# Kernel tuning notes

Measured on AMD Instinct MI355X. Metric: run time of the kernel, lower is better.

The kernel has to match this reference:

```python
import jax, jax.numpy as jnp
import numpy as np

FACTOR = 1.0

def _dct_matrix():
    n = 8
    D = np.zeros((n * n, n * n), dtype=np.float32)
    for u in range(n):
        for v in range(n):
            au = 1.0 / np.sqrt(2.0) if u == 0 else 1.0
            av = 1.0 / np.sqrt(2.0) if v == 0 else 1.0
            alpha = au * av * 0.25
            for x in range(n):
                for y in range(n):
                    D[u * n + v, x * n + y] = alpha * np.cos((2 * x + 1) * u * np.pi / 16) * np.cos((2 * y + 1) * v * np.pi / 16)
    return D

def _y_quant_table():
    t = np.array([[16, 11, 10, 16, 24, 40, 51, 61], [12, 12, 14, 19, 26, 58, 60, 55],
                  [14, 13, 16, 24, 40, 57, 69, 56], [14, 17, 22, 29, 51, 87, 80, 62],
                  [18, 22, 37, 56, 68, 109, 103, 77], [24, 35, 55, 64, 81, 104, 113, 92],
                  [49, 64, 78, 87, 103, 121, 120, 101], [72, 92, 95, 98, 112, 100, 103, 99]],
                 dtype=np.float32).T
    return t

def _c_quant_table():
    t = np.full((8, 8), 99, dtype=np.float32)
    t[:4, :4] = np.array([[17, 18, 24, 47], [18, 21, 26, 66], [24, 26, 56, 99], [47, 66, 99, 99]],
                          dtype=np.float32).T
    return t

_D = jnp.asarray(_dct_matrix())          # [64,64]
_QT = jnp.stack([jnp.asarray(_y_quant_table()),
                 jnp.asarray(_c_quant_table()),
                 jnp.asarray(_c_quant_table())], axis=0) * FACTOR  # [3,8,8]

def setup_inputs() -> dict:
    key = jax.random.key(0)
    image = jax.random.uniform(key, (32, 3, 512, 512), dtype=jnp.float32)
    return {"image": image}

def _diffjpeg(image):
    x = jnp.clip(image, 0.0, 1.0)
    B, C, H, W = x.shape  # H, W multiples of 8 -> no padding branch
    r, g, b = x[:, 0], x[:, 1], x[:, 2]
    y = 0.299 * r + 0.587 * g + 0.114 * b
    cb = (b - y) * 0.564 + 0.5
    cr = (r - y) * 0.713 + 0.5
    ycbcr = jnp.stack([y, cb, cr], axis=1)  # [B,3,H,W]
    # blockify into 8x8 tiles
    nh, nw = H // 8, W // 8
    blocks = ycbcr.reshape(B, C, nh, 8, nw, 8).transpose(0, 1, 2, 4, 3, 5)  # [B,C,nh,nw,8,8]
    flat = blocks.reshape(-1, 64) * 255.0 - 128.0
    dct = flat @ _D.T                      # matmul(D, flat.T).T
    dctb = dct.reshape(B, C, nh, nw, 8, 8)
    qte = _QT[None, :, None, None, :, :]   # [1,3,1,1,8,8]
    q = dctb / qte
    q = q + jax.lax.stop_gradient(jnp.round(q) - q)  # STE rounding
    deq = q * qte
    idct = deq.reshape(-1, 64) @ _D        # matmul(D.T, x.T).T
    idct = (idct + 128.0) / 255.0
    img = idct.reshape(B, C, nh, nw, 8, 8).transpose(0, 1, 2, 4, 3, 5).reshape(B, C, H, W)
    yy, ycb, ycr = img[:, 0], img[:, 1] - 0.5, img[:, 2] - 0.5
    rr = yy + 1.403 * ycr
    gg = yy - 0.714 * ycr - 0.344 * ycb
    bb = yy + 1.773 * ycb
    rgb = jnp.clip(jnp.stack([rr, gg, bb], axis=1), 0.0, 1.0)
    return jnp.clip(rgb, 0.0, 1.0)

def reference(image):
    return _diffjpeg(image)
```

## Files before the change

kernel.cpp:

```cpp
#include <hip/hip_runtime.h>

#define K4 0.353553391f
#define K1 0.490392640f
#define K3 0.415734806f
#define K5 0.277785117f
#define K7 0.097545161f
#define K2 0.461939766f
#define K6 0.191341716f

__device__ __align__(16) const float YQT[64] = {
    16.f, 12.f, 14.f, 14.f,  18.f,  24.f,  49.f,  72.f,
    11.f, 12.f, 13.f, 17.f,  22.f,  35.f,  64.f,  92.f,
    10.f, 14.f, 16.f, 22.f,  37.f,  55.f,  78.f,  95.f,
    16.f, 19.f, 24.f, 29.f,  56.f,  64.f,  87.f,  98.f,
    24.f, 26.f, 40.f, 51.f,  68.f,  81.f, 103.f, 112.f,
    40.f, 58.f, 57.f, 87.f, 109.f, 104.f, 121.f, 100.f,
    51.f, 60.f, 69.f, 80.f, 103.f, 113.f, 120.f, 103.f,
    61.f, 55.f, 56.f, 62.f,  77.f,  92.f, 101.f,  99.f
};

__device__ __align__(16) const float CQ[64] = {
    17.f, 18.f, 24.f, 47.f, 99.f, 99.f, 99.f, 99.f,
    18.f, 21.f, 26.f, 66.f, 99.f, 99.f, 99.f, 99.f,
    24.f, 26.f, 56.f, 99.f, 99.f, 99.f, 99.f, 99.f,
    47.f, 66.f, 99.f, 99.f, 99.f, 99.f, 99.f, 99.f,
    99.f, 99.f, 99.f, 99.f, 99.f, 99.f, 99.f, 99.f,
    99.f, 99.f, 99.f, 99.f, 99.f, 99.f, 99.f, 99.f,
    99.f, 99.f, 99.f, 99.f, 99.f, 99.f, 99.f, 99.f,
    99.f, 99.f, 99.f, 99.f, 99.f, 99.f, 99.f, 99.f
};

__device__ __forceinline__ void dct8(const float x[8], float X[8]) {
    const float a0 = x[0] + x[7], a1 = x[1] + x[6], a2 = x[2] + x[5], a3 = x[3] + x[4];
    const float d0 = x[0] - x[7], d1 = x[1] - x[6], d2 = x[2] - x[5], d3 = x[3] - x[4];
    const float e0 = a0 + a3, e1 = a1 + a2, f0 = a0 - a3, f1 = a1 - a2;
    X[0] = K4 * (e0 + e1);
    X[4] = K4 * (e0 - e1);
    X[2] = K2 * f0 + K6 * f1;
    X[6] = K6 * f0 - K2 * f1;
    X[1] = K1 * d0 + K3 * d1 + K5 * d2 + K7 * d3;
    X[3] = K3 * d0 - K7 * d1 - K1 * d2 - K5 * d3;
    X[5] = K5 * d0 - K1 * d1 + K7 * d2 + K3 * d3;
    X[7] = K7 * d0 - K5 * d1 + K3 * d2 - K1 * d3;
}

__device__ __forceinline__ void idct8(const float X[8], float x[8]) {
    const float g0 = K4 * (X[0] + X[4]);
    const float g1 = K4 * (X[0] - X[4]);
    const float E0 = g0 + K2 * X[2] + K6 * X[6];
    const float E1 = g1 + K6 * X[2] - K2 * X[6];
    const float E2 = g1 - K6 * X[2] + K2 * X[6];
    const float E3 = g0 - K2 * X[2] - K6 * X[6];
    const float O0 = K1 * X[1] + K3 * X[3] + K5 * X[5] + K7 * X[7];
    const float O1 = K3 * X[1] - K7 * X[3] - K1 * X[5] - K5 * X[7];
    const float O2 = K5 * X[1] - K1 * X[3] + K7 * X[5] + K3 * X[7];
    const float O3 = K7 * X[1] - K5 * X[3] + K3 * X[5] - K1 * X[7];
    x[0] = E0 + O0;  x[7] = E0 - O0;
    x[1] = E1 + O1;  x[6] = E1 - O1;
    x[2] = E2 + O2;  x[5] = E2 - O2;
    x[3] = E3 + O3;  x[4] = E3 - O3;
}

__device__ __forceinline__ void wave_lds_fence() {
    asm volatile("s_waitcnt lgkmcnt(0)" ::: "memory");
}

#define LDSW 68

__global__ __launch_bounds__(256, 6) void diffjpeg_kernel(const float* __restrict__ in,
                                                          float* __restrict__ out)
{
    __shared__ __align__(16) float pl[3][32][LDSW];

    const int t  = threadIdx.x;
    const int l  = t & 63;
    const int wv = t >> 6;
    const int r0 = wv * 8;

    const int bid  = blockIdx.x;
    const int img  = bid >> 7;
    const int rem  = bid & 127;
    const int trow = rem >> 3;
    const int tcol = rem & 7;
    const size_t HW = (size_t)512 * 512;
    const size_t sbase = (size_t)img * 3 * HW + (size_t)(trow * 32 + wv * 8) * 512 + (size_t)(tcol * 64);
    const float* __restrict__ pin  = in  + sbase;
    float* __restrict__       pout = out + sbase;

    {
        const float* cb = pin + l;
        float rv[8], gv[8], bv[8];
        #pragma unroll
        for (int x = 0; x < 8; ++x) rv[x] = cb[(size_t)x * 512];
        #pragma unroll
        for (int x = 0; x < 8; ++x) gv[x] = cb[HW + (size_t)x * 512];
        #pragma unroll
        for (int x = 0; x < 8; ++x) bv[x] = cb[2 * HW + (size_t)x * 512];

        float yv[8], cbv[8], crv[8];
        #pragma unroll
        for (int x = 0; x < 8; ++x) {
            const float r = fminf(fmaxf(rv[x], 0.f), 1.f);
            const float g = fminf(fmaxf(gv[x], 0.f), 1.f);
            const float b = fminf(fmaxf(bv[x], 0.f), 1.f);
            const float Y = fmaf(76.245f, r, fmaf(149.685f, g, 29.07f * b));
            yv[x]  = Y - 128.f;
            cbv[x] = fmaf(0.564f, fmaf(255.f, b, -Y), -0.5f);
            crv[x] = fmaf(0.713f, fmaf(255.f, r, -Y), -0.5f);
        }

        float X0[8], X1[8], X2[8];
        dct8(yv,  X0);
        dct8(cbv, X1);
        dct8(crv, X2);
        #pragma unroll
        for (int u = 0; u < 8; ++u) {
            pl[0][r0 + u][l] = X0[u];
            pl[1][r0 + u][l] = X1[u];
            pl[2][r0 + u][l] = X2[u];
        }
    }
    wave_lds_fence();

    {
        const int b8 = (l >> 3) * 8;
        const int rr = l & 7;

        const float4* yq4 = (const float4*)&YQT[rr * 8];
        const float4* cq4 = (const float4*)&CQ[rr * 8];
        const float4 yqa = yq4[0], yqb = yq4[1];
        const float4 cqa = cq4[0], cqb = cq4[1];
        const float yq[8] = {yqa.x, yqa.y, yqa.z, yqa.w, yqb.x, yqb.y, yqb.z, yqb.w};
        const float cq[8] = {cqa.x, cqa.y, cqa.z, cqa.w, cqb.x, cqb.y, cqb.z, cqb.w};

        #pragma unroll
        for (int c = 0; c < 3; ++c) {
            float4* rp = (float4*)&pl[c][r0 + rr][b8];
            const float4 a0 = rp[0];
            const float4 a1 = rp[1];
            const float T[8] = {a0.x, a0.y, a0.z, a0.w, a1.x, a1.y, a1.z, a1.w};
            float S[8];
            dct8(T, S);
            float Dq[8];
            #pragma unroll
            for (int v = 0; v < 8; ++v) {
                const float qt = (c == 0) ? yq[v] : cq[v];
                Dq[v] = rintf(S[v] / qt) * qt;
            }
            float o[8];
            idct8(Dq, o);
            rp[0] = make_float4(o[0], o[1], o[2], o[3]);
            rp[1] = make_float4(o[4], o[5], o[6], o[7]);
        }
    }
    wave_lds_fence();

    {
        float Xy[8], Xcb[8], Xcr[8];
        #pragma unroll
        for (int u = 0; u < 8; ++u) {
            Xy[u]  = pl[0][r0 + u][l];
            Xcb[u] = pl[1][r0 + u][l];
            Xcr[u] = pl[2][r0 + u][l];
        }
        float sy[8], scb[8], scr[8];
        idct8(Xy,  sy);
        idct8(Xcb, scb);
        idct8(Xcr, scr);

        float* ob = pout + l;
        constexpr float inv255 = 1.0f / 255.0f;
        constexpr float Kr = 0.504711754f;
        constexpr float Kg = 0.499886280f;
        constexpr float Kb = 0.505437240f;
        #pragma unroll
        for (int x = 0; x < 8; ++x) {
            const float rr = fmaf(inv255, fmaf(1.403f, scr[x], sy[x]), Kr);
            const float tg = fmaf(-0.714f, scr[x], fmaf(-0.344f, scb[x], sy[x]));
            const float gg = fmaf(inv255, tg, Kg);
            const float bb = fmaf(inv255, fmaf(1.773f, scb[x], sy[x]), Kb);
            __builtin_nontemporal_store(fminf(fmaxf(rr, 0.f), 1.f), ob + (size_t)x * 512);
            __builtin_nontemporal_store(fminf(fmaxf(gg, 0.f), 1.f), ob + HW + (size_t)x * 512);
            __builtin_nontemporal_store(fminf(fmaxf(bb, 0.f), 1.f), ob + 2 * HW + (size_t)x * 512);
        }
    }
}

extern "C" void kernel_launch(void* const* d_in, const int* in_sizes, int n_in,
                              void* d_out, int out_size, void* d_ws, size_t ws_size,
                              hipStream_t stream) {
    const float* in = (const float*)d_in[0];
    float* out = (float*)d_out;
    const int B = in_sizes[0] / (3 * 512 * 512);
    const int grid = B * 128;
    diffjpeg_kernel<<<grid, 256, 0, stream>>>(in, out);
}
```

Before: 37.38 us.

## Pack chroma channels into float2 for packed FMA and replace division with reciprocal

Processes the Cb and Cr channels together as two-wide float vectors so the DCT, IDCT and color-conversion arithmetic can map to packed FP32 instructions (v_pk_fma_f32) on CDNA. The per-coefficient division during quantization is replaced by multiplication with precomputed reciprocal tables plus one Newton-style correction FMA to keep the result close to true division before rounding. This aims to cut VALU instruction count in a kernel that may be partly compute-bound. The cost is extra constant-table loads and possible register or shuffle overhead from packing and unpacking. The correction step carries a small risk of rounding ties differing from exact division.

```diff
diff --git a/kernel.cpp b/kernel.cpp
--- a/kernel.cpp
+++ b/kernel.cpp
@@ -1,4 +1,6 @@
 #include <hip/hip_runtime.h>
+
+typedef float f32x2 __attribute__((ext_vector_type(2)));
 
 #define K4 0.353553391f
 #define K1 0.490392640f
@@ -18,7 +20,16 @@
     51.f, 60.f, 69.f, 80.f, 103.f, 113.f, 120.f, 103.f,
     61.f, 55.f, 56.f, 62.f,  77.f,  92.f, 101.f,  99.f
 };
-
+__device__ __align__(16) const float RYQT[64] = {
+    1.f/16.f, 1.f/12.f, 1.f/14.f, 1.f/14.f, 1.f/18.f,  1.f/24.f,  1.f/49.f,  1.f/72.f,
+    1.f/11.f, 1.f/12.f, 1.f/13.f, 1.f/17.f, 1.f/22.f,  1.f/35.f,  1.f/64.f,  1.f/92.f,
+    1.f/10.f, 1.f/14.f, 1.f/16.f, 1.f/22.f, 1.f/37.f,  1.f/55.f,  1.f/78.f,  1.f/95.f,
+    1.f/16.f, 1.f/19.f, 1.f/24.f, 1.f/29.f, 1.f/56.f,  1.f/64.f,  1.f/87.f,  1.f/98.f,
+    1.f/24.f, 1.f/26.f, 1.f/40.f, 1.f/51.f, 1.f/68.f,  1.f/81.f,  1.f/103.f, 1.f/112.f,
+    1.f/40.f, 1.f/58.f, 1.f/57.f, 1.f/87.f, 1.f/109.f, 1.f/104.f, 1.f/121.f, 1.f/100.f,
+    1.f/51.f, 1.f/60.f, 1.f/69.f, 1.f/80.f, 1.f/103.f, 1.f/113.f, 1.f/120.f, 1.f/103.f,
+    1.f/61.f, 1.f/55.f, 1.f/56.f, 1.f/62.f, 1.f/77.f,  1.f/92.f,  1.f/101.f, 1.f/99.f
+};
 __device__ __align__(16) const float CQ[64] = {
     17.f, 18.f, 24.f, 47.f, 99.f, 99.f, 99.f, 99.f,
     18.f, 21.f, 26.f, 66.f, 99.f, 99.f, 99.f, 99.f,
@@ -29,36 +40,60 @@
     99.f, 99.f, 99.f, 99.f, 99.f, 99.f, 99.f, 99.f,
     99.f, 99.f, 99.f, 99.f, 99.f, 99.f, 99.f, 99.f
 };
-
-__device__ __forceinline__ void dct8(const float x[8], float X[8]) {
-    const float a0 = x[0] + x[7], a1 = x[1] + x[6], a2 = x[2] + x[5], a3 = x[3] + x[4];
-    const float d0 = x[0] - x[7], d1 = x[1] - x[6], d2 = x[2] - x[5], d3 = x[3] - x[4];
-    const float e0 = a0 + a3, e1 = a1 + a2, f0 = a0 - a3, f1 = a1 - a2;
+__device__ __align__(16) const float RCQ[64] = {
+    1.f/17.f, 1.f/18.f, 1.f/24.f, 1.f/47.f, 1.f/99.f, 1.f/99.f, 1.f/99.f, 1.f/99.f,
+    1.f/18.f, 1.f/21.f, 1.f/26.f, 1.f/66.f, 1.f/99.f, 1.f/99.f, 1.f/99.f, 1.f/99.f,
+    1.f/24.f, 1.f/26.f, 1.f/56.f, 1.f/99.f, 1.f/99.f, 1.f/99.f, 1.f/99.f, 1.f/99.f,
+    1.f/47.f, 1.f/66.f, 1.f/99.f, 1.f/99.f, 1.f/99.f, 1.f/99.f, 1.f/99.f, 1.f/99.f,
+    1.f/99.f, 1.f/99.f, 1.f/99.f, 1.f/99.f, 1.f/99.f, 1.f/99.f, 1.f/99.f, 1.f/99.f,
+    1.f/99.f, 1.f/99.f, 1.f/99.f, 1.f/99.f, 1.f/99.f, 1.f/99.f, 1.f/99.f, 1.f/99.f,
+    1.f/99.f, 1.f/99.f, 1.f/99.f, 1.f/99.f, 1.f/99.f, 1.f/99.f, 1.f/99.f, 1.f/99.f,
+    1.f/99.f, 1.f/99.f, 1.f/99.f, 1.f/99.f, 1.f/99.f, 1.f/99.f, 1.f/99.f, 1.f/99.f
+};
+
+__device__ __forceinline__ float gfma(float a, float b, float c) { return fmaf(a, b, c); }
+__device__ __forceinline__ f32x2 gfma(f32x2 a, f32x2 b, f32x2 c) { return __builtin_elementwise_fma(a, b, c); }
+__device__ __forceinline__ f32x2 gfma(float a, f32x2 b, f32x2 c) { return __builtin_elementwise_fma((f32x2){a, a}, b, c); }
+
+template <typename T>
+__device__ __forceinline__ void dct8(const T x[8], T X[8]) {
+    const T a0 = x[0] + x[7], a1 = x[1] + x[6], a2 = x[2] + x[5], a3 = x[3] + x[4];
+    const T d0 = x[0] - x[7], d1 = x[1] - x[6], d2 = x[2] - x[5], d3 = x[3] - x[4];
+    const T e0 = a0 + a3, e1 = a1 + a2, f0 = a0 - a3, f1 = a1 - a2;
     X[0] = K4 * (e0 + e1);
     X[4] = K4 * (e0 - e1);
-    X[2] = K2 * f0 + K6 * f1;
-    X[6] = K6 * f0 - K2 * f1;
-    X[1] = K1 * d0 + K3 * d1 + K5 * d2 + K7 * d3;
-    X[3] = K3 * d0 - K7 * d1 - K1 * d2 - K5 * d3;
-    X[5] = K5 * d0 - K1 * d1 + K7 * d2 + K3 * d3;
-    X[7] = K7 * d0 - K5 * d1 + K3 * d2 - K1 * d3;
-}
-
-__device__ __forceinline__ void idct8(const float X[8], float x[8]) {
-    const float g0 = K4 * (X[0] + X[4]);
-    const float g1 = K4 * (X[0] - X[4]);
-    const float E0 = g0 + K2 * X[2] + K6 * X[6];
-    const float E1 = g1 + K6 * X[2] - K2 * X[6];
-    const float E2 = g1 - K6 * X[2] + K2 * X[6];
-    const float E3 = g0 - K2 * X[2] - K6 * X[6];
-    const float O0 = K1 * X[1] + K3 * X[3] + K5 * X[5] + K7 * X[7];
-    const float O1 = K3 * X[1] - K7 * X[3] - K1 * X[5] - K5 * X[7];
-    const float O2 = K5 * X[1] - K1 * X[3] + K7 * X[5] + K3 * X[7];
-    const float O3 = K7 * X[1] - K5 * X[3] + K3 * X[5] - K1 * X[7];
+    X[2] = gfma(K6, f1, K2 * f0);
+    X[6] = gfma(-K2, f1, K6 * f0);
+    X[1] = gfma(K7, d3, gfma(K5, d2, gfma(K3, d1, K1 * d0)));
+    X[3] = gfma(-K5, d3, gfma(-K1, d2, gfma(-K7, d1, K3 * d0)));
+    X[5] = gfma(K3, d3, gfma(K7, d2, gfma(-K1, d1, K5 * d0)));
+    X[7] = gfma(-K1, d3, gfma(K3, d2, gfma(-K5, d1, K7 * d0)));
+}
+
+template <typename T>
+__device__ __forceinline__ void idct8(const T X[8], T x[8]) {
+    const T g0 = K4 * (X[0] + X[4]);
+    const T g1 = K4 * (X[0] - X[4]);
+    const T E0 = gfma(K6, X[6], gfma(K2, X[2], g0));
+    const T E1 = gfma(-K2, X[6], gfma(K6, X[2], g1));
+    const T E2 = gfma(K2, X[6], gfma(-K6, X[2], g1));
+    const T E3 = gfma(-K6, X[6], gfma(-K2, X[2], g0));
+    const T O0 = gfma(K7, X[7], gfma(K5, X[5], gfma(K3, X[3], K1 * X[1])));
+    const T O1 = gfma(-K5, X[7], gfma(-K1, X[5], gfma(-K7, X[3], K3 * X[1])));
+    const T O2 = gfma(K3, X[7], gfma(K7, X[5], gfma(-K1, X[3], K5 * X[1])));
+    const T O3 = gfma(-K1, X[7], gfma(K3, X[5], gfma(-K5, X[3], K7 * X[1])));
     x[0] = E0 + O0;  x[7] = E0 - O0;
     x[1] = E1 + O1;  x[6] = E1 - O1;
     x[2] = E2 + O2;  x[5] = E2 - O2;
     x[3] = E3 + O3;  x[4] = E3 - O3;
+}
+
+__device__ __forceinline__ f32x2 quant2(f32x2 sv, f32x2 qt, f32x2 rq) {
+    const f32x2 q0 = sv * rq;
+    const f32x2 e  = gfma(-qt, q0, sv);
+    const f32x2 q  = gfma(rq, e, q0);
+    const f32x2 n  = {rintf(q.x), rintf(q.y)};
+    return n * qt;
 }
 
 __device__ __forceinline__ void wave_lds_fence() {
@@ -97,27 +132,28 @@
         #pragma unroll
         for (int x = 0; x < 8; ++x) bv[x] = cb[2 * HW + (size_t)x * 512];
 
-        float yv[8], cbv[8], crv[8];
+        float yv[8];
+        f32x2 cc[8];
         #pragma unroll
         for (int x = 0; x < 8; ++x) {
             const float r = fminf(fmaxf(rv[x], 0.f), 1.f);
             const float g = fminf(fmaxf(gv[x], 0.f), 1.f);
             const float b = fminf(fmaxf(bv[x], 0.f), 1.f);
             const float Y = fmaf(76.245f, r, fmaf(149.685f, g, 29.07f * b));
-            yv[x]  = Y - 128.f;
-            cbv[x] = fmaf(0.564f, fmaf(255.f, b, -Y), -0.5f);
-            crv[x] = fmaf(0.713f, fmaf(255.f, r, -Y), -0.5f);
-        }
-
-        float X0[8], X1[8], X2[8];
-        dct8(yv,  X0);
-        dct8(cbv, X1);
-        dct8(crv, X2);
+            yv[x] = Y - 128.f;
+            const f32x2 tbr = gfma(255.f, (f32x2){b, r}, (f32x2){-Y, -Y});
+            cc[x] = gfma((f32x2){0.564f, 0.713f}, tbr, (f32x2){-0.5f, -0.5f});
+        }
+
+        float X0[8];
+        f32x2 XC[8];
+        dct8(yv, X0);
+        dct8(cc, XC);
         #pragma unroll
         for (int u = 0; u < 8; ++u) {
             pl[0][r0 + u][l] = X0[u];
-            pl[1][r0 + u][l] = X1[u];
-            pl[2][r0 + u][l] = X2[u];
+            pl[1][r0 + u][l] = XC[u].x;
+            pl[2][r0 + u][l] = XC[u].y;
         }
     }
     wave_lds_fence();
@@ -126,16 +162,21 @@
         const int b8 = (l >> 3) * 8;
         const int rr = l & 7;
 
-        const float4* yq4 = (const float4*)&YQT[rr * 8];
-        const float4* cq4 = (const float4*)&CQ[rr * 8];
-        const float4 yqa = yq4[0], yqb = yq4[1];
-        const float4 cqa = cq4[0], cqb = cq4[1];
-        const float yq[8] = {yqa.x, yqa.y, yqa.z, yqa.w, yqb.x, yqb.y, yqb.z, yqb.w};
-        const float cq[8] = {cqa.x, cqa.y, cqa.z, cqa.w, cqb.x, cqb.y, cqb.z, cqb.w};
-
-        #pragma unroll
-        for (int c = 0; c < 3; ++c) {
-            float4* rp = (float4*)&pl[c][r0 + rr][b8];
+        const float4* yq4  = (const float4*)&YQT[rr * 8];
+        const float4* ryq4 = (const float4*)&RYQT[rr * 8];
+        const float4* cq4  = (const float4*)&CQ[rr * 8];
+        const float4* rcq4 = (const float4*)&RCQ[rr * 8];
+        const float4 yqa = yq4[0],  yqb = yq4[1];
+        const float4 rya = ryq4[0], ryb = ryq4[1];
+        const float4 cqa = cq4[0],  cqb = cq4[1];
+        const float4 rca = rcq4[0], rcb4 = rcq4[1];
+        const float yq[8]  = {yqa.x, yqa.y, yqa.z, yqa.w, yqb.x, yqb.y, yqb.z, yqb.w};
+        const float ryq[8] = {rya.x, rya.y, rya.z, rya.w, ryb.x, ryb.y, ryb.z, ryb.w};
+        const float cq[8]  = {cqa.x, cqa.y, cqa.z, cqa.w, cqb.x, cqb.y, cqb.z, cqb.w};
+        const float rcq[8] = {rca.x, rca.y, rca.z, rca.w, rcb4.x, rcb4.y, rcb4.z, rcb4.w};
+
+        {
+            float4* rp = (float4*)&pl[0][r0 + rr][b8];
             const float4 a0 = rp[0];
             const float4 a1 = rp[1];
             const float T[8] = {a0.x, a0.y, a0.z, a0.w, a1.x, a1.y, a1.z, a1.w};
@@ -143,30 +184,53 @@
             dct8(T, S);
             float Dq[8];
             #pragma unroll
-            for (int v = 0; v < 8; ++v) {
-                const float qt = (c == 0) ? yq[v] : cq[v];
-                Dq[v] = rintf(S[v] / qt) * qt;
+            for (int i = 0; i < 4; ++i) {
+                const f32x2 d = quant2((f32x2){S[2*i], S[2*i+1]},
+                                       (f32x2){yq[2*i], yq[2*i+1]},
+                                       (f32x2){ryq[2*i], ryq[2*i+1]});
+                Dq[2*i] = d.x; Dq[2*i+1] = d.y;
             }
             float o[8];
             idct8(Dq, o);
             rp[0] = make_float4(o[0], o[1], o[2], o[3]);
             rp[1] = make_float4(o[4], o[5], o[6], o[7]);
         }
+
+        {
+            float4* rpb = (float4*)&pl[1][r0 + rr][b8];
+            float4* rpr = (float4*)&pl[2][r0 + rr][b8];
+            const float4 c0 = rpb[0], c1 = rpb[1];
+            const float4 e0 = rpr[0], e1 = rpr[1];
+            const f32x2 T[8] = {{c0.x, e0.x}, {c0.y, e0.y}, {c0.z, e0.z}, {c0.w, e0.w},
+                                {c1.x, e1.x}, {c1.y, e1.y}, {c1.z, e1.z}, {c1.w, e1.w}};
+            f32x2 S[8];
+            dct8(T, S);
+            f32x2 Dq[8];
+            #pragma unroll
+            for (int v = 0; v < 8; ++v)
+                Dq[v] = quant2(S[v], (f32x2){cq[v], cq[v]}, (f32x2){rcq[v], rcq[v]});
+            f32x2 o[8];
+            idct8(Dq, o);
+            rpb[0] = make_float4(o[0].x, o[1].x, o[2].x, o[3].x);
+            rpb[1] = make_float4(o[4].x, o[5].x, o[6].x, o[7].x);
+            rpr[0] = make_float4(o[0].y, o[1].y, o[2].y, o[3].y);
+            rpr[1] = make_float4(o[4].y, o[5].y, o[6].y, o[7].y);
+        }
     }
     wave_lds_fence();
 
     {
-        float Xy[8], Xcb[8], Xcr[8];
+        float Xy[8];
+        f32x2 Xc[8];
         #pragma unroll
         for (int u = 0; u < 8; ++u) {
-            Xy[u]  = pl[0][r0 + u][l];
-            Xcb[u] = pl[1][r0 + u][l];
-            Xcr[u] = pl[2][r0 + u][l];
-        }
-        float sy[8], scb[8], scr[8];
-        idct8(Xy,  sy);
-        idct8(Xcb, scb);
-        idct8(Xcr, scr);
+            Xy[u] = pl[0][r0 + u][l];
+            Xc[u] = (f32x2){pl[1][r0 + u][l], pl[2][r0 + u][l]};
+        }
+        float sy[8];
+        f32x2 sc[8];
+        idct8(Xy, sy);
+        idct8(Xc, sc);
 
         float* ob = pout + l;
         constexpr float inv255 = 1.0f / 255.0f;
@@ -175,13 +239,15 @@
         constexpr float Kb = 0.505437240f;
         #pragma unroll
         for (int x = 0; x < 8; ++x) {
-            const float rr = fmaf(inv255, fmaf(1.403f, scr[x], sy[x]), Kr);
-            const float tg = fmaf(-0.714f, scr[x], fmaf(-0.344f, scb[x], sy[x]));
-            const float gg = fmaf(inv255, tg, Kg);
-            const float bb = fmaf(inv255, fmaf(1.773f, scb[x], sy[x]), Kb);
-            __builtin_nontemporal_store(fminf(fmaxf(rr, 0.f), 1.f), ob + (size_t)x * 512);
-            __builtin_nontemporal_store(fminf(fmaxf(gg, 0.f), 1.f), ob + HW + (size_t)x * 512);
-            __builtin_nontemporal_store(fminf(fmaxf(bb, 0.f), 1.f), ob + 2 * HW + (size_t)x * 512);
+            const float scb = sc[x].x;
+            const float scr = sc[x].y;
+            const f32x2 inner = gfma((f32x2){1.403f, 1.773f}, (f32x2){scr, scb},
+                                     (f32x2){sy[x], sy[x]});
+            const f32x2 rb = gfma(inv255, inner, (f32x2){Kr, Kb});
+            const float gg = fmaf(inv255, fmaf(-0.714f, scr, fmaf(-0.344f, scb, sy[x])), Kg);
+            __builtin_nontemporal_store(fminf(fmaxf(rb.x, 0.f), 1.f), ob + (size_t)x * 512);
+            __builtin_nontemporal_store(fminf(fmaxf(gg,   0.f), 1.f), ob + HW + (size_t)x * 512);
+            __builtin_nontemporal_store(fminf(fmaxf(rb.y, 0.f), 1.f), ob + 2 * HW + (size_t)x * 512);
         }
     }
 }
```

Result: faster. 35.50 us (-5.0%).
